# Performance work log

Hardware: AMD Instinct MI355X
Metric: run time of the kernel (lower is better)

The kernel has to match this reference:

```python
import jax, jax.numpy as jnp
import numpy as np
from jax import lax

SLOPE = 25.0  # snntorch surrogate.fast_sigmoid default slope
NUM_STEPS = 25

@jax.custom_vjp
def spike_fn(x):
    # forward: heaviside(x > 0); backward: fast-sigmoid surrogate grad
    return (x > 0).astype(x.dtype)

def _spike_fwd(x):
    return spike_fn(x), x

def _spike_bwd(x, g):
    return (g / (SLOPE * jnp.abs(x) + 1.0) ** 2,)

spike_fn.defvjp(_spike_fwd, _spike_bwd)


def setup_inputs() -> dict:
    key = jax.random.key(0)
    ks = jax.random.split(key, 6)
    B, NI, NH, NO = 32768, 256, 1024, 1
    x = jax.random.normal(ks[0], (B, NI), dtype=jnp.float32)
    W1 = jax.random.normal(ks[1], (NH, NI), dtype=jnp.float32) / np.sqrt(NI)
    b1 = jax.random.normal(ks[2], (NH,), dtype=jnp.float32) * 0.01
    W2 = jax.random.normal(ks[3], (NO, NH), dtype=jnp.float32) / np.sqrt(NH)
    b2 = jax.random.normal(ks[4], (NO,), dtype=jnp.float32) * 0.01
    beta = jnp.asarray(0.9, dtype=jnp.float32)       # learn_beta=True scalar
    thr = jnp.full((NH,), 1.0, dtype=jnp.float32)    # learn_threshold=True
    return {"x": x, "W1": W1, "b1": b1, "W2": W2, "b2": b2, "beta": beta, "thr": thr}


def reference(x, W1, b1, W2, b2, beta, thr):
    x1 = x @ W1.T + b1                      # [B, NH], constant input each step
    beta_c = jnp.clip(beta, 0.0, 1.0)

    def step(carry, _):
        mem, spk_sum = carry
        reset = spike_fn(mem - thr)         # reset based on previous membrane
        mem_new = beta_c * mem + x1 - reset * thr  # subtract reset mechanism
        spk = spike_fn(mem_new - thr)
        return (mem_new, spk_sum + spk), None

    init = (jnp.zeros_like(x1), jnp.zeros_like(x1))
    (mem, spk_sum), _ = lax.scan(step, init, None, length=NUM_STEPS)
    return spk_sum @ W2.T + b2              # [B, 1]
```

## Files before the change

### kernel.cpp

```cpp
#include <hip/hip_runtime.h>


#define NI 256
#define NH 1024
#define NSTEPS 25
#define BT 128
#define BK 32
#define NTILES (NI / BK)
#define BPROW 132
#define RW 40

typedef _Float16 half8 __attribute__((ext_vector_type(8)));
typedef _Float16 half4 __attribute__((ext_vector_type(4)));
typedef float float4v __attribute__((ext_vector_type(4)));

__device__ __forceinline__ unsigned f2k(float f) {
    unsigned u = __float_as_uint(f);
    return (u >> 31) ? ~u : (u | 0x80000000u);
}
__device__ __forceinline__ float k2f(unsigned k) {
    unsigned u = (k & 0x80000000u) ? (k & 0x7FFFFFFFu) : ~k;
    return __uint_as_float(u);
}

__device__ __forceinline__ int lif_count(float x1, float beta, float th) {
    float mem = 0.f;
    float spk = (0.f > th) ? 1.f : 0.f;
    int c = 0;
#pragma unroll
    for (int t = 0; t < NSTEPS; t++) {
        mem = fmaf(spk, -th, fmaf(beta, mem, x1));
        spk = (mem > th) ? 1.f : 0.f;
        c += (mem > th);
    }
    return c;
}

__device__ __forceinline__ void split8(const float* src, half8* hi, half8* lo) {
    float4v a = *(const float4v*)src;
    float4v b = *(const float4v*)(src + 4);
#pragma unroll
    for (int e = 0; e < 4; e++) {
        _Float16 h = (_Float16)a[e];
        (*hi)[e] = h;
        (*lo)[e] = (_Float16)(a[e] - (float)h);
        h = (_Float16)b[e];
        (*hi)[e + 4] = h;
        (*lo)[e + 4] = (_Float16)(b[e] - (float)h);
    }
}


__global__ __launch_bounds__(256) void snn_prep(
    const float* __restrict__ x, const float* __restrict__ W1,
    const float* __restrict__ thr, const float* __restrict__ betap,
    const float* __restrict__ b2, float* __restrict__ out,
    float* __restrict__ bp, _Float16* __restrict__ whp, _Float16* __restrict__ wlp,
    _Float16* __restrict__ xhp, _Float16* __restrict__ xlp, int B)
{
    const int tid = threadIdx.x;
    const int XB = B / 8;
    int bid = blockIdx.x;

    if (bid < XB) {
        const int G = bid * 256 + tid;
        const int band = G >> 12;
        const int rem = G & 4095;
        const int kt = rem >> 9;
        const int rem2 = rem & 511;
        const int r8 = rem2 >> 6, quad = (rem2 >> 4) & 3, col = rem2 & 15;
        const float* src = x + (size_t)(band * 128 + r8 * 16 + col) * NI + kt * 32 + quad * 8;
        half8 hi, lo;
        split8(src, &hi, &lo);
        ((half8*)xhp)[G] = hi;
        ((half8*)xlp)[G] = lo;
        return;
    }
    bid -= XB;
    if (bid < 128) {
        const int G = bid * 256 + tid;
        const int band = G >> 12;
        const int rem = G & 4095;
        const int kt = rem >> 9;
        const int rem2 = rem & 511;
        const int r8 = rem2 >> 6, quad = (rem2 >> 4) & 3, col = rem2 & 15;
        const float* src = W1 + (size_t)(band * 128 + r8 * 16 + col) * NI + kt * 32 + quad * 8;
        half8 hi, lo;
        split8(src, &hi, &lo);
        ((half8*)whp)[G] = hi;
        ((half8*)wlp)[G] = lo;
        return;
    }
    bid -= 128;
    if (bid < 100) {
        const int idx = bid * 256 + tid;
        const int h = idx / NSTEPS;
        const int k = idx % NSTEPS + 1;
        const float th = thr[h];
        float beta = betap[0];
        beta = beta < 0.f ? 0.f : (beta > 1.f ? 1.f : beta);
        unsigned lo = f2k(-3.0e38f), hi = f2k(3.0e38f);
        float res;
        if (lif_count(k2f(hi), beta, th) < k) {
            res = 3.0e38f;
        } else if (lif_count(k2f(lo), beta, th) >= k) {
            res = -3.0e38f;
        } else {
#pragma unroll 1
            for (int it = 0; it < 32; it++) {
                unsigned mid = lo + ((hi - lo) >> 1);
                if (lif_count(k2f(mid), beta, th) >= k) hi = mid; else lo = mid;
            }
            res = k2f(hi);
        }
        bp[(k - 1) * NH + h] = res;
        return;
    }
    bid -= 100;
    {
        const int i = bid * 256 + tid;
        if (i < B) out[i] = b2[0];
    }
}

__global__ __launch_bounds__(256, 2) void snn_main_fast(
    const _Float16* __restrict__ xhp, const _Float16* __restrict__ xlp,
    const _Float16* __restrict__ whp, const _Float16* __restrict__ wlp,
    const float* __restrict__ b1, const float* __restrict__ W2,
    const float* __restrict__ bp, float* __restrict__ out)
{
    __shared__ float smem[128 * 33];

    const int tid  = threadIdx.x;
    const int w    = tid >> 6;
    const int lane = tid & 63;
    const int col  = lane & 15;
    const int quad = lane >> 4;
    const int wbb  = (w >> 1) * 64;
    const int whh  = (w & 1) * 64;
    const int r8x0 = (w >> 1) * 4;
    const int r8w0 = (w & 1) * 4;
    const int bband = blockIdx.x;
    const int hband = blockIdx.y;
    const int b0 = bband * BT;
    const int h0 = hband * BT;
    const int loff = quad * 16 + col;

    const half8* xh = (const half8*)xhp + (size_t)bband * 4096;
    const half8* xl = (const half8*)xlp + (size_t)bband * 4096;
    const half8* wh = (const half8*)whp + (size_t)hband * 4096;
    const half8* wl = (const half8*)wlp + (size_t)hband * 4096;

    float4v acc[4][4];
#pragma unroll
    for (int i = 0; i < 4; i++)
#pragma unroll
        for (int j = 0; j < 4; j++) acc[i][j] = (float4v){0.f, 0.f, 0.f, 0.f};

#pragma unroll 2
    for (int kt = 0; kt < NTILES; kt++) {
        const int xi = kt * 512 + r8x0 * 64 + loff;
        const int wi = kt * 512 + r8w0 * 64 + loff;
        half8 ah[4], al[4], bh[4], bl[4];
#pragma unroll
        for (int i = 0; i < 4; i++) {
            ah[i] = xh[xi + i * 64];
            al[i] = xl[xi + i * 64];
        }
#pragma unroll
        for (int j = 0; j < 4; j++) {
            bh[j] = wh[wi + j * 64];
            bl[j] = wl[wi + j * 64];
        }
#pragma unroll
        for (int j = 0; j < 4; j++)
#pragma unroll
            for (int i = 0; i < 4; i++) {
                acc[i][j] = __builtin_amdgcn_mfma_f32_16x16x32_f16(ah[i], bh[j], acc[i][j], 0, 0, 0);
                acc[i][j] = __builtin_amdgcn_mfma_f32_16x16x32_f16(ah[i], bl[j], acc[i][j], 0, 0, 0);
                acc[i][j] = __builtin_amdgcn_mfma_f32_16x16x32_f16(al[i], bh[j], acc[i][j], 0, 0, 0);
            }
    }

    float* bpl = smem;
    for (int n = tid; n < 31 * 128; n += 256) {
        const int t = n >> 7, hl = n & 127;
        bpl[t * BPROW + hl] = (t < NSTEPS) ? bp[t * NH + h0 + hl] : 3.0e38f;
    }
    __syncthreads();

    float part[16];
#pragma unroll
    for (int e = 0; e < 16; e++) part[e] = 0.f;

#pragma unroll
    for (int j = 0; j < 4; j++) {
        const int hl = whh + 16 * j + col;
        const int h = h0 + hl;
        const float w2 = W2[h];
        const float bj = b1[h];
        const float* pj = bpl + hl;
        float x1[16];
        int mo[16];
#pragma unroll
        for (int e = 0; e < 16; e++) {
            x1[e] = acc[e >> 2][j][e & 3] + bj;
            mo[e] = 0;
        }
#pragma unroll
        for (int bstep = 16; bstep >= 1; bstep >>= 1) {
#pragma unroll
            for (int e = 0; e < 16; e++) {
                const float c = pj[mo[e] + (bstep - 1) * BPROW];
                mo[e] += (x1[e] >= c) ? bstep * BPROW : 0;
            }
        }
#pragma unroll
        for (int e = 0; e < 16; e++) {
            const float cntf = (float)mo[e] * (1.0f / BPROW);
            part[e] = fmaf(cntf, w2, part[e]);
        }
    }

    __syncthreads();
    float* red = smem;
#pragma unroll
    for (int e = 0; e < 16; e++) {
        const int row = wbb + 16 * (e >> 2) + 4 * quad + (e & 3);
        red[row * 33 + (w & 1) * 16 + col] = part[e];
    }
    __syncthreads();
    if (tid < BT) {
        float s = 0.f;
#pragma unroll
        for (int c = 0; c < 32; c++) s += red[tid * 33 + c];
        atomicAdd(&out[b0 + tid], s);
    }
}


__global__ __launch_bounds__(256) void snn_prep_small(
    const float* __restrict__ thr, const float* __restrict__ betap,
    const float* __restrict__ b2, float* __restrict__ out,
    float* __restrict__ bp, int B)
{
    const int tid = threadIdx.x;
    int bid = blockIdx.x;
    if (bid < 100) {
        const int idx = bid * 256 + tid;
        const int h = idx / NSTEPS;
        const int k = idx % NSTEPS + 1;
        const float th = thr[h];
        float beta = betap[0];
        beta = beta < 0.f ? 0.f : (beta > 1.f ? 1.f : beta);
        unsigned lo = f2k(-3.0e38f), hi = f2k(3.0e38f);
        float res;
        if (lif_count(k2f(hi), beta, th) < k) res = 3.0e38f;
        else if (lif_count(k2f(lo), beta, th) >= k) res = -3.0e38f;
        else {
#pragma unroll 1
            for (int it = 0; it < 32; it++) {
                unsigned mid = lo + ((hi - lo) >> 1);
                if (lif_count(k2f(mid), beta, th) >= k) hi = mid; else lo = mid;
            }
            res = k2f(hi);
        }
        bp[(k - 1) * NH + h] = res;
        return;
    }
    bid -= 100;
    const int i = bid * 256 + tid;
    if (i < B) out[i] = b2[0];
}

__global__ __launch_bounds__(256, 3) void snn_main_fb(
    const float* __restrict__ x, const float* __restrict__ W1,
    const float* __restrict__ b1, const float* __restrict__ W2,
    const float* __restrict__ bp, float* __restrict__ out)
{
    __shared__ __align__(16) _Float16 lds[4 * BT * RW];
    _Float16* xh = lds;
    _Float16* xl = lds + BT * RW;
    _Float16* wh = lds + 2 * BT * RW;
    _Float16* wl = lds + 3 * BT * RW;

    const int tid  = threadIdx.x;
    const int w    = tid >> 6;
    const int lane = tid & 63;
    const int col  = lane & 15;
    const int quad = lane >> 4;
    const int wbb  = (w >> 1) * 64;
    const int whh  = (w & 1) * 64;
    const int b0 = blockIdx.x * BT;
    const int h0 = blockIdx.y * BT;

    float4v acc[4][4];
#pragma unroll
    for (int i = 0; i < 4; i++)
#pragma unroll
        for (int j = 0; j < 4; j++) acc[i][j] = (float4v){0.f, 0.f, 0.f, 0.f};

    const int r0 = tid >> 3;
    const int c4 = tid & 7;
    const float* xrow = x + (size_t)(b0 + r0) * NI + 4 * c4;
    const float* wrow = W1 + (size_t)(h0 + r0) * NI + 4 * c4;

    for (int kt = 0; kt < NTILES; kt++) {
        const int ko = kt * BK;
        float4v vx[4], vw[4];
#pragma unroll
        for (int p = 0; p < 4; p++) {
            vx[p] = *(const float4v*)(xrow + (size_t)(32 * p) * NI + ko);
            vw[p] = *(const float4v*)(wrow + (size_t)(32 * p) * NI + ko);
        }
        __syncthreads();
#pragma unroll
        for (int p = 0; p < 4; p++) {
            const int row = r0 + 32 * p;
            half4 hx, lx, hw, lw;
#pragma unroll
            for (int q = 0; q < 4; q++) {
                float v = vx[p][q];
                _Float16 h = (_Float16)v;
                hx[q] = h;
                lx[q] = (_Float16)(v - (float)h);
                v = vw[p][q];
                h = (_Float16)v;
                hw[q] = h;
                lw[q] = (_Float16)(v - (float)h);
            }
            *(half4*)&xh[row * RW + 4 * c4] = hx;
            *(half4*)&xl[row * RW + 4 * c4] = lx;
            *(half4*)&wh[row * RW + 4 * c4] = hw;
            *(half4*)&wl[row * RW + 4 * c4] = lw;
        }
        __syncthreads();

        half8 ah[4], al[4];
#pragma unroll
        for (int i = 0; i < 4; i++) {
            ah[i] = *(const half8*)&xh[(wbb + 16 * i + col) * RW + 8 * quad];
            al[i] = *(const half8*)&xl[(wbb + 16 * i + col) * RW + 8 * quad];
        }
#pragma unroll
        for (int j = 0; j < 4; j++) {
            half8 bh = *(const half8*)&wh[(whh + 16 * j + col) * RW + 8 * quad];
            half8 bl = *(const half8*)&wl[(whh + 16 * j + col) * RW + 8 * quad];
#pragma unroll
            for (int i = 0; i < 4; i++) {
                acc[i][j] = __builtin_amdgcn_mfma_f32_16x16x32_f16(ah[i], bh, acc[i][j], 0, 0, 0);
                acc[i][j] = __builtin_amdgcn_mfma_f32_16x16x32_f16(ah[i], bl, acc[i][j], 0, 0, 0);
                acc[i][j] = __builtin_amdgcn_mfma_f32_16x16x32_f16(al[i], bh, acc[i][j], 0, 0, 0);
            }
        }
    }

    __syncthreads();
    float* bpl = (float*)lds;
    for (int n = tid; n < NSTEPS * 128; n += 256)
        bpl[n] = bp[(n >> 7) * NH + h0 + (n & 127)];
    __syncthreads();

    float part[16];
#pragma unroll
    for (int e = 0; e < 16; e++) part[e] = 0.f;
#pragma unroll
    for (int j = 0; j < 4; j++) {
        const int hl = whh + 16 * j + col;
        const int h = h0 + hl;
        const float w2 = W2[h];
        const float bj = b1[h];
        float x1[16];
        int cnt[16];
#pragma unroll
        for (int e = 0; e < 16; e++) {
            x1[e] = acc[e >> 2][j][e & 3] + bj;
            cnt[e] = 0;
        }
#pragma unroll
        for (int k = 0; k < NSTEPS; k++) {
            const float c = bpl[k * 128 + hl];
#pragma unroll
            for (int e = 0; e < 16; e++) cnt[e] += (x1[e] >= c) ? 1 : 0;
        }
#pragma unroll
        for (int e = 0; e < 16; e++)
            part[e] = fmaf((float)cnt[e], w2, part[e]);
    }

    __syncthreads();
    float* red = (float*)lds;
#pragma unroll
    for (int e = 0; e < 16; e++) {
        const int row = wbb + 16 * (e >> 2) + 4 * quad + (e & 3);
        red[row * 33 + (w & 1) * 16 + col] = part[e];
    }
    __syncthreads();
    if (tid < BT) {
        float s = 0.f;
#pragma unroll
        for (int c = 0; c < 32; c++) s += red[tid * 33 + c];
        atomicAdd(&out[b0 + tid], s);
    }
}

extern "C" void kernel_launch(void* const* d_in, const int* in_sizes, int n_in,
                              void* d_out, int out_size, void* d_ws, size_t ws_size,
                              hipStream_t stream) {
    const float* x    = (const float*)d_in[0];
    const float* W1   = (const float*)d_in[1];
    const float* b1   = (const float*)d_in[2];
    const float* W2   = (const float*)d_in[3];
    const float* b2   = (const float*)d_in[4];
    const float* beta = (const float*)d_in[5];
    const float* thr  = (const float*)d_in[6];
    float* out = (float*)d_out;

    const int B = in_sizes[0] / NI;

    char* ws = (char*)d_ws;
    float*     bp  = (float*)ws;
    size_t off = (size_t)NH * NSTEPS * 4;
    _Float16* whp = (_Float16*)(ws + off);  off += (size_t)NH * NI * 2;
    _Float16* wlp = (_Float16*)(ws + off);  off += (size_t)NH * NI * 2;
    _Float16* xhp = (_Float16*)(ws + off);  off += (size_t)B * NI * 2;
    _Float16* xlp = (_Float16*)(ws + off);  off += (size_t)B * NI * 2;
    const size_t ws_need = off;

    if (ws_size >= ws_need) {
        const int nblk = B / 8 + 128 + 100 + (B + 255) / 256;
        snn_prep<<<nblk, 256, 0, stream>>>(x, W1, thr, beta, b2, out,
                                           bp, whp, wlp, xhp, xlp, B);
        dim3 grid(B / BT, NH / BT);
        snn_main_fast<<<grid, 256, 0, stream>>>(xhp, xlp, whp, wlp, b1, W2, bp, out);
    } else {
        snn_prep_small<<<100 + (B + 255) / 256, 256, 0, stream>>>(thr, beta, b2, out, bp, B);
        dim3 grid(B / BT, NH / BT);
        snn_main_fb<<<grid, 256, 0, stream>>>(x, W1, b1, W2, bp, out);
    }
}
```

Measured before the change: 168.7 us.

## Prefetch MFMA operands, fold bias into thresholds, linear-count spikes from registers

The GEMM loop now double-buffers its half8 operand loads in registers: tile kt+1 is fetched while tile kt's MFMAs run, and the loop is fully unrolled. The per-neuron spike thresholds are precomputed with b1 folded in, stored h-major with a stride of 32, and copied into shared memory before the GEMM rather than after it. The shared-memory binary search per element is replaced by a linear count over 25 thresholds held in registers. Together these aim to hide global load latency and remove dependent LDS lookups, in exchange for more register pressure and more compare instructions.

Result: slower. 189.0 us (+12.0%).

```diff
diff --git a/kernel.cpp b/kernel.cpp
--- a/kernel.cpp
+++ b/kernel.cpp
@@ -7,7 +7,7 @@
 #define BT 128
 #define BK 32
 #define NTILES (NI / BK)
-#define BPROW 132
+#define BPR 36
 #define RW 40
 
 typedef _Float16 half8 __attribute__((ext_vector_type(8)));
@@ -54,8 +54,9 @@
 __global__ __launch_bounds__(256) void snn_prep(
     const float* __restrict__ x, const float* __restrict__ W1,
     const float* __restrict__ thr, const float* __restrict__ betap,
-    const float* __restrict__ b2, float* __restrict__ out,
-    float* __restrict__ bp, _Float16* __restrict__ whp, _Float16* __restrict__ wlp,
+    const float* __restrict__ b1, const float* __restrict__ b2,
+    float* __restrict__ out, float* __restrict__ bp,
+    _Float16* __restrict__ whp, _Float16* __restrict__ wlp,
     _Float16* __restrict__ xhp, _Float16* __restrict__ xlp, int B)
 {
     const int tid = threadIdx.x;
@@ -97,23 +98,24 @@
         const int h = idx / NSTEPS;
         const int k = idx % NSTEPS + 1;
         const float th = thr[h];
+        const float bj = b1[h];
         float beta = betap[0];
         beta = beta < 0.f ? 0.f : (beta > 1.f ? 1.f : beta);
         unsigned lo = f2k(-3.0e38f), hi = f2k(3.0e38f);
         float res;
-        if (lif_count(k2f(hi), beta, th) < k) {
+        if (lif_count(k2f(hi) + bj, beta, th) < k) {
             res = 3.0e38f;
-        } else if (lif_count(k2f(lo), beta, th) >= k) {
+        } else if (lif_count(k2f(lo) + bj, beta, th) >= k) {
             res = -3.0e38f;
         } else {
 #pragma unroll 1
             for (int it = 0; it < 32; it++) {
                 unsigned mid = lo + ((hi - lo) >> 1);
-                if (lif_count(k2f(mid), beta, th) >= k) hi = mid; else lo = mid;
+                if (lif_count(k2f(mid) + bj, beta, th) >= k) hi = mid; else lo = mid;
             }
             res = k2f(hi);
         }
-        bp[(k - 1) * NH + h] = res;
+        bp[h * 32 + (k - 1)] = res;
         return;
     }
     bid -= 100;
@@ -126,10 +128,10 @@
 __global__ __launch_bounds__(256, 2) void snn_main_fast(
     const _Float16* __restrict__ xhp, const _Float16* __restrict__ xlp,
     const _Float16* __restrict__ whp, const _Float16* __restrict__ wlp,
-    const float* __restrict__ b1, const float* __restrict__ W2,
-    const float* __restrict__ bp, float* __restrict__ out)
+    const float* __restrict__ W2, const float* __restrict__ bp,
+    float* __restrict__ out)
 {
-    __shared__ float smem[128 * 33];
+    __shared__ float smem[128 * BPR];
 
     const int tid  = threadIdx.x;
     const int w    = tid >> 6;
@@ -138,18 +140,26 @@
     const int quad = lane >> 4;
     const int wbb  = (w >> 1) * 64;
     const int whh  = (w & 1) * 64;
-    const int r8x0 = (w >> 1) * 4;
-    const int r8w0 = (w & 1) * 4;
     const int bband = blockIdx.x;
     const int hband = blockIdx.y;
     const int b0 = bband * BT;
     const int h0 = hband * BT;
     const int loff = quad * 16 + col;
 
-    const half8* xh = (const half8*)xhp + (size_t)bband * 4096;
-    const half8* xl = (const half8*)xlp + (size_t)bband * 4096;
-    const half8* wh = (const half8*)whp + (size_t)hband * 4096;
-    const half8* wl = (const half8*)wlp + (size_t)hband * 4096;
+    const half8* xh = (const half8*)xhp + (size_t)bband * 4096 + (w >> 1) * 256 + loff;
+    const half8* xl = (const half8*)xlp + (size_t)bband * 4096 + (w >> 1) * 256 + loff;
+    const half8* wh = (const half8*)whp + (size_t)hband * 4096 + (w & 1) * 256 + loff;
+    const half8* wl = (const half8*)wlp + (size_t)hband * 4096 + (w & 1) * 256 + loff;
+
+    float* bpl = smem;
+    {
+        const int hl = tid >> 1, q = (tid & 1) * 4;
+#pragma unroll
+        for (int rep = 0; rep < 4; rep++) {
+            float4v v = *(const float4v*)&bp[(h0 + hl) * 32 + q + 8 * rep];
+            *(float4v*)&bpl[hl * BPR + q + 8 * rep] = v;
+        }
+    }
 
     float4v acc[4][4];
 #pragma unroll
@@ -157,36 +167,44 @@
 #pragma unroll
         for (int j = 0; j < 4; j++) acc[i][j] = (float4v){0.f, 0.f, 0.f, 0.f};
 
-#pragma unroll 2
+    half8 cah[4], cal[4], cbh[4], cbl[4];
+#pragma unroll
+    for (int i = 0; i < 4; i++) {
+        cah[i] = xh[i * 64];
+        cal[i] = xl[i * 64];
+        cbh[i] = wh[i * 64];
+        cbl[i] = wl[i * 64];
+    }
+#pragma unroll
     for (int kt = 0; kt < NTILES; kt++) {
-        const int xi = kt * 512 + r8x0 * 64 + loff;
-        const int wi = kt * 512 + r8w0 * 64 + loff;
-        half8 ah[4], al[4], bh[4], bl[4];
-#pragma unroll
-        for (int i = 0; i < 4; i++) {
-            ah[i] = xh[xi + i * 64];
-            al[i] = xl[xi + i * 64];
-        }
-#pragma unroll
-        for (int j = 0; j < 4; j++) {
-            bh[j] = wh[wi + j * 64];
-            bl[j] = wl[wi + j * 64];
+        half8 nah[4], nal[4], nbh[4], nbl[4];
+        if (kt < NTILES - 1) {
+            const int nx = (kt + 1) * 512;
+#pragma unroll
+            for (int i = 0; i < 4; i++) {
+                nah[i] = xh[nx + i * 64];
+                nal[i] = xl[nx + i * 64];
+                nbh[i] = wh[nx + i * 64];
+                nbl[i] = wl[nx + i * 64];
+            }
         }
 #pragma unroll
         for (int j = 0; j < 4; j++)
 #pragma unroll
             for (int i = 0; i < 4; i++) {
-                acc[i][j] = __builtin_amdgcn_mfma_f32_16x16x32_f16(ah[i], bh[j], acc[i][j], 0, 0, 0);
-                acc[i][j] = __builtin_amdgcn_mfma_f32_16x16x32_f16(ah[i], bl[j], acc[i][j], 0, 0, 0);
-                acc[i][j] = __builtin_amdgcn_mfma_f32_16x16x32_f16(al[i], bh[j], acc[i][j], 0, 0, 0);
-            }
-    }
-
-    float* bpl = smem;
-    for (int n = tid; n < 31 * 128; n += 256) {
-        const int t = n >> 7, hl = n & 127;
-        bpl[t * BPROW + hl] = (t < NSTEPS) ? bp[t * NH + h0 + hl] : 3.0e38f;
-    }
+                acc[i][j] = __builtin_amdgcn_mfma_f32_16x16x32_f16(cah[i], cbh[j], acc[i][j], 0, 0, 0);
+                acc[i][j] = __builtin_amdgcn_mfma_f32_16x16x32_f16(cah[i], cbl[j], acc[i][j], 0, 0, 0);
+                acc[i][j] = __builtin_amdgcn_mfma_f32_16x16x32_f16(cal[i], cbh[j], acc[i][j], 0, 0, 0);
+            }
+        if (kt < NTILES - 1) {
+#pragma unroll
+            for (int i = 0; i < 4; i++) {
+                cah[i] = nah[i]; cal[i] = nal[i];
+                cbh[i] = nbh[i]; cbl[i] = nbl[i];
+            }
+        }
+    }
+
     __syncthreads();
 
     float part[16];
@@ -196,30 +214,27 @@
 #pragma unroll
     for (int j = 0; j < 4; j++) {
         const int hl = whh + 16 * j + col;
-        const int h = h0 + hl;
-        const float w2 = W2[h];
-        const float bj = b1[h];
-        const float* pj = bpl + hl;
+        const float w2 = W2[h0 + hl];
+        float4v c[7];
+#pragma unroll
+        for (int q = 0; q < 7; q++)
+            c[q] = *(const float4v*)&bpl[hl * BPR + 4 * q];
         float x1[16];
-        int mo[16];
+        int cnt[16];
 #pragma unroll
         for (int e = 0; e < 16; e++) {
-            x1[e] = acc[e >> 2][j][e & 3] + bj;
-            mo[e] = 0;
-        }
-#pragma unroll
-        for (int bstep = 16; bstep >= 1; bstep >>= 1) {
-#pragma unroll
-            for (int e = 0; e < 16; e++) {
-                const float c = pj[mo[e] + (bstep - 1) * BPROW];
-                mo[e] += (x1[e] >= c) ? bstep * BPROW : 0;
-            }
-        }
-#pragma unroll
-        for (int e = 0; e < 16; e++) {
-            const float cntf = (float)mo[e] * (1.0f / BPROW);
-            part[e] = fmaf(cntf, w2, part[e]);
-        }
+            x1[e] = acc[e >> 2][j][e & 3];
+            cnt[e] = 0;
+        }
+#pragma unroll
+        for (int k = 0; k < NSTEPS; k++) {
+            const float ck = c[k >> 2][k & 3];
+#pragma unroll
+            for (int e = 0; e < 16; e++) cnt[e] += (x1[e] >= ck) ? 1 : 0;
+        }
+#pragma unroll
+        for (int e = 0; e < 16; e++)
+            part[e] = fmaf((float)cnt[e], w2, part[e]);
     }
 
     __syncthreads();
@@ -233,7 +248,7 @@
     if (tid < BT) {
         float s = 0.f;
 #pragma unroll
-        for (int c = 0; c < 32; c++) s += red[tid * 33 + c];
+        for (int c2 = 0; c2 < 32; c2++) s += red[tid * 33 + c2];
         atomicAdd(&out[b0 + tid], s);
     }
 }
@@ -420,7 +435,7 @@
 
     char* ws = (char*)d_ws;
     float*     bp  = (float*)ws;
-    size_t off = (size_t)NH * NSTEPS * 4;
+    size_t off = (size_t)NH * 32 * 4;
     _Float16* whp = (_Float16*)(ws + off);  off += (size_t)NH * NI * 2;
     _Float16* wlp = (_Float16*)(ws + off);  off += (size_t)NH * NI * 2;
     _Float16* xhp = (_Float16*)(ws + off);  off += (size_t)B * NI * 2;
@@ -429,10 +444,10 @@
 
     if (ws_size >= ws_need) {
         const int nblk = B / 8 + 128 + 100 + (B + 255) / 256;
-        snn_prep<<<nblk, 256, 0, stream>>>(x, W1, thr, beta, b2, out,
+        snn_prep<<<nblk, 256, 0, stream>>>(x, W1, thr, beta, b1, b2, out,
                                            bp, whp, wlp, xhp, xlp, B);
         dim3 grid(B / BT, NH / BT);
-        snn_main_fast<<<grid, 256, 0, stream>>>(xhp, xlp, whp, wlp, b1, W2, bp, out);
+        snn_main_fast<<<grid, 256, 0, stream>>>(xhp, xlp, whp, wlp, W2, bp, out);
     } else {
         snn_prep_small<<<100 + (B + 255) / 256, 256, 0, stream>>>(thr, beta, b2, out, bp, B);
         dim3 grid(B / BT, NH / BT);
```
